# Performance work log

Measured on AMD Instinct MI355X. Metric: run time of the kernel, lower is better.

The kernel has to match this reference:

```python
import jax, jax.numpy as jnp
import numpy as np

B, A, NN, G, F, L, MAXZ = 8, 1024, 64, 25, 128, 3, 100
CUTOFF = 5.0

def ssp(x):
    # shifted softplus: ln(0.5*e^x + 0.5) = softplus(x) - ln(2)
    return jax.nn.softplus(x) - jnp.log(2.0)

def setup_inputs() -> dict:
    key = jax.random.key(0)
    ks = jax.random.split(key, 10)
    atomic_numbers = jax.random.randint(ks[0], (B, A), 0, MAXZ)
    positions = jax.random.normal(ks[1], (B, A, 3), dtype=jnp.float32) * 3.0
    cell = jnp.zeros((B, 3, 3), dtype=jnp.float32)
    cell_offset = jnp.zeros((B, A, NN, 3), dtype=jnp.float32)
    neighbors = jax.random.randint(ks[2], (B, A, NN), 0, A)
    neighbor_mask = jnp.ones((B, A, NN), dtype=jnp.float32)
    s = 0.05
    emb = jax.random.normal(ks[3], (MAXZ, F), dtype=jnp.float32) * s
    emb = emb.at[0].set(0.0)  # padding_idx=0
    return dict(
        atomic_numbers=atomic_numbers, positions=positions, cell=cell,
        cell_offset=cell_offset, neighbors=neighbors, neighbor_mask=neighbor_mask,
        emb=emb,
        fw1=jax.random.normal(ks[4], (L, G, F), dtype=jnp.float32) * s,
        fb1=jnp.zeros((L, F), dtype=jnp.float32),
        fw2=jax.random.normal(ks[5], (L, F, F), dtype=jnp.float32) * s,
        fb2=jnp.zeros((L, F), dtype=jnp.float32),
        in2f_w=jax.random.normal(ks[6], (L, F, F), dtype=jnp.float32) * s,
        f2out_w=jax.random.normal(ks[7], (L, F, F), dtype=jnp.float32) * s,
        f2out_b=jnp.zeros((L, F), dtype=jnp.float32),
        dense_w=jax.random.normal(ks[8], (L, F, F), dtype=jnp.float32) * s,
        dense_b=jnp.zeros((L, F), dtype=jnp.float32),
    )

def reference(atomic_numbers, positions, cell, cell_offset, neighbors,
              neighbor_mask, emb, fw1, fb1, fw2, fb2, in2f_w, f2out_w,
              f2out_b, dense_w, dense_b):
    bidx = jnp.arange(B)[:, None, None]
    # embedding lookup [B,A,F]
    x = emb[atomic_numbers]
    # AtomDistances: gather neighbor positions, add cell offsets, norm
    pos_j = positions[bidx, neighbors]                       # [B,A,NN,3]
    dv = pos_j - positions[:, :, None, :] + jnp.einsum('bank,bkc->banc', cell_offset, cell)
    d2 = jnp.sum(dv * dv, axis=-1)                           # [B,A,NN]
    r_ij = jnp.where(d2 > 0, jnp.sqrt(jnp.where(d2 > 0, d2, 1.0)), 0.0)
    # GaussianSmearing on [0, cutoff] with G gaussians
    offsets = jnp.linspace(0.0, CUTOFF, G)
    width = offsets[1] - offsets[0]
    coeff = -0.5 / (width * width)
    f_ij = jnp.exp(coeff * (r_ij[..., None] - offsets) ** 2)  # [B,A,NN,G]
    mask = neighbor_mask[..., None]                           # [B,A,NN,1]
    for l in range(L):
        # filter-generating network on expanded distances -> [B,A,NN,F]
        W = ssp(f_ij @ fw1[l] + fb1[l]) @ fw2[l] + fb2[l]
        # cfconv: in2f (no bias), gather neighbor features, mul, masked sum
        y = x @ in2f_w[l]                                     # [B,A,F]
        yj = y[bidx, neighbors]                               # [B,A,NN,F]
        v = jnp.sum(yj * W * mask, axis=2)                    # [B,A,F]
        v = ssp(v @ f2out_w[l] + f2out_b[l])
        # interaction output dense (linear)
        v = v @ dense_w[l] + dense_b[l]
        x = x + v
    return x
```

## Files before the change

kernel.cpp:

```cpp
#include <hip/hip_runtime.h>
#include <hip/hip_bf16.h>
#include <math.h>

#define B_ 8
#define A_ 1024
#define NN_ 64
#define G_ 25
#define F_ 128
#define L_ 3
#define TG_ 4096

typedef __hip_bfloat16 bf16;
typedef __bf16 bf16x8 __attribute__((ext_vector_type(8)));
typedef __bf16 bf16x4 __attribute__((ext_vector_type(4)));
typedef float floatx4 __attribute__((ext_vector_type(4)));
#define MFMA16 __builtin_amdgcn_mfma_f32_16x16x32_bf16

__device__ __forceinline__ float sspfast(float x){
  return __logf(0.5f*__expf(x) + 0.5f);
}
__device__ __forceinline__ float ldsel(const void* p, long long i, int isbf){
  return isbf ? __bfloat162float(((const bf16*)p)[i]) : ((const float*)p)[i];
}
__device__ __forceinline__ int sniff_bf16(const void* pos){
  const unsigned* raw = (const unsigned*)pos;
  unsigned w = raw[threadIdx.x & 63];
  unsigned e = (w >> 7) & 0xFF;
  return __popcll(__ballot(e >= 118 && e <= 132)) >= 32;
}

__global__ __launch_bounds__(256) void k_setup(
    const void* emb, const void* fb1, const void* fb2, const void* f2ob,
    const void* db,  const void* fw1, const void* fw2, const void* f2ow,
    const void* dw,  const void* in2f, const void* pos,
    float* c_emb, float* c_fb1, float* c_fb2, float* c_f2ob, float* c_db,
    __bf16* fw1tb, __bf16* fw2tb, __bf16* f2owtb, __bf16* dwtb, __bf16* in2ftb)
{
  int isbf = sniff_bf16(pos);
  int idx = blockIdx.x*256 + threadIdx.x;
  if(idx < 12800){ c_emb[idx] = ldsel(emb, idx, isbf); return; }
  if(idx < 13184){ c_fb1[idx-12800] = ldsel(fb1, idx-12800, isbf); return; }
  if(idx < 13568){ c_fb2[idx-13184] = ldsel(fb2, idx-13184, isbf); return; }
  if(idx < 13952){ c_f2ob[idx-13568] = ldsel(f2ob, idx-13568, isbf); return; }
  if(idx < 14336){ c_db[idx-13952] = ldsel(db, idx-13952, isbf); return; }
  if(idx < 26624){
    int i = idx - 14336;
    int l = i >> 12; int rem = i & 4095; int f = rem >> 5; int k = rem & 31;
    float v = (k < G_) ? ldsel(fw1, (long long)l*G_*F_ + k*F_ + f, isbf) : 0.0f;
    fw1tb[i] = (__bf16)v;
    return;
  }
  {
    int i = idx - 26624;
    int which = i / 49152; int r = i - which*49152;
    int l = r >> 14; int rem = r & 16383; int f = rem >> 7; int k = rem & 127;
    const void* src = (which==0) ? fw2 : (which==1) ? f2ow : (which==2) ? dw : in2f;
    __bf16* dst = (which==0) ? fw2tb : (which==1) ? f2owtb : (which==2) ? dwtb : in2ftb;
    dst[r] = (__bf16)ldsel(src, (long long)l*F_*F_ + k*F_ + f, isbf);
  }
}

__global__ __launch_bounds__(256, 4) void k_build(
    const __bf16* __restrict__ fw1tb, const float* __restrict__ fb1g,
    const __bf16* __restrict__ fw2tb, const float* __restrict__ fb2g,
    __bf16* __restrict__ wtabb,
    const int* __restrict__ z, const float* __restrict__ c_emb,
    const __bf16* __restrict__ in2ftb, float* __restrict__ xws,
    __bf16* __restrict__ ybf,
    const void* pos, const void* cell, const void* celloff,
    const int* __restrict__ nbr, const void* maskg,
    int4* __restrict__ pair)
{
  __shared__ __align__(16) unsigned char smem[22528];
  int t = threadIdx.x;
  int lane = t & 63, wid = t >> 6, c = lane & 15, quad = lane >> 4;
  int wb = wid*32;

  if(blockIdx.x >= 448){
    int isbf = sniff_bf16(pos);
    int p = (blockIdx.x - 448)*256 + t;
    int m = p >> 6;
    int b = m >> 10;
    int j = nbr[p];
    long long pi = (long long)m*3, pj = (long long)(b*A_+j)*3;
    long long co = (long long)p*3, ce = (long long)b*9;
    float o0 = ldsel(celloff,co+0,isbf), o1 = ldsel(celloff,co+1,isbf), o2 = ldsel(celloff,co+2,isbf);
    float d2 = 0.0f;
    #pragma unroll
    for(int cc=0;cc<3;cc++){
      float off = o0*ldsel(cell,ce+cc,isbf) + o1*ldsel(cell,ce+3+cc,isbf) + o2*ldsel(cell,ce+6+cc,isbf);
      float dv = ldsel(pos,pj+cc,isbf) - ldsel(pos,pi+cc,isbf) + off;
      d2 += dv*dv;
    }
    float r = (d2 > 0.0f) ? sqrtf(d2) : 0.0f;
    float msk = ldsel(maskg, p, isbf);
    int i = (int)(r * ((float)TG_ / 8.0f) + 0.5f);
    if(i > TG_-1) i = TG_-1;
    int4 pr;
    pr.x = i * F_;
    pr.y = (b*A_ + j) * F_;
    pr.z = __float_as_int(msk);
    pr.w = 0;
    pair[p] = pr;
    return;
  }

  if(blockIdx.x < 192){
    __bf16* s_h1  = (__bf16*)smem;
    __bf16* s_fij = (__bf16*)(smem + 17408);
    int layer = blockIdx.x >> 6;
    int row0  = (blockIdx.x & 63) * 64;

    const float dr = 8.0f / (float)TG_;
    const float width = 5.0f/24.0f;
    const float coeff = -0.5f/(width*width);
    for(int i=t;i<NN_*40;i+=256){
      int n = i/40, g = i - n*40;
      float val = 0.0f;
      if(g < G_){
        float rg = (float)(row0 + n) * dr;
        float d = rg - (float)g*width;
        val = __expf(coeff*d*d);
      }
      s_fij[i] = (__bf16)val;
    }
    __syncthreads();

    {
      const __bf16* fw1l = fw1tb + layer*F_*32;
      bf16x8 a0 = *(const bf16x8*)(fw1l + (wb + c)*32 + quad*8);
      bf16x8 a1 = *(const bf16x8*)(fw1l + (wb + 16 + c)*32 + quad*8);
      floatx4 bias0 = *(const floatx4*)(fb1g + layer*F_ + wb + quad*4);
      floatx4 bias1 = *(const floatx4*)(fb1g + layer*F_ + wb + 16 + quad*4);
      #pragma unroll
      for(int nt=0;nt<4;nt++){
        bf16x8 bfr = *(const bf16x8*)(s_fij + (nt*16 + c)*40 + quad*8);
        floatx4 z4 = {0.f,0.f,0.f,0.f};
        floatx4 acc0 = MFMA16(a0, bfr, z4, 0,0,0);
        floatx4 acc1 = MFMA16(a1, bfr, z4, 0,0,0);
        bf16x4 h0, h1v;
        #pragma unroll
        for(int r=0;r<4;r++){
          h0[r]  = (__bf16)sspfast(acc0[r] + bias0[r]);
          h1v[r] = (__bf16)sspfast(acc1[r] + bias1[r]);
        }
        *(bf16x4*)(s_h1 + (nt*16+c)*136 + wb + quad*4)      = h0;
        *(bf16x4*)(s_h1 + (nt*16+c)*136 + wb + 16 + quad*4) = h1v;
      }
    }
    __syncthreads();

    {
      const __bf16* fw2l = fw2tb + layer*F_*F_;
      bf16x8 aw0[4], aw1[4];
      #pragma unroll
      for(int kt=0;kt<4;kt++){
        aw0[kt] = *(const bf16x8*)(fw2l + (wb + c)*F_ + kt*32 + quad*8);
        aw1[kt] = *(const bf16x8*)(fw2l + (wb + 16 + c)*F_ + kt*32 + quad*8);
      }
      floatx4 ba0 = *(const floatx4*)(fb2g + layer*F_ + wb + quad*4);
      floatx4 ba1 = *(const floatx4*)(fb2g + layer*F_ + wb + 16 + quad*4);
      __bf16* T = wtabb + (long long)layer*TG_*F_;
      #pragma unroll
      for(int nt=0; nt<4; nt++){
        bf16x8 bh[4];
        #pragma unroll
        for(int kt=0;kt<4;kt++)
          bh[kt] = *(const bf16x8*)(s_h1 + (nt*16 + c)*136 + kt*32 + quad*8);
        floatx4 acc0 = {0.f,0.f,0.f,0.f};
        floatx4 acc1 = {0.f,0.f,0.f,0.f};
        #pragma unroll
        for(int kt=0;kt<4;kt++){
          acc0 = MFMA16(aw0[kt], bh[kt], acc0, 0,0,0);
          acc1 = MFMA16(aw1[kt], bh[kt], acc1, 0,0,0);
        }
        int row = row0 + nt*16 + c;
        bf16x4 o0, o1;
        #pragma unroll
        for(int r=0;r<4;r++){
          o0[r] = (__bf16)(acc0[r] + ba0[r]);
          o1[r] = (__bf16)(acc1[r] + ba1[r]);
        }
        *(bf16x4*)(T + (long long)row*F_ + wb + quad*4)      = o0;
        *(bf16x4*)(T + (long long)row*F_ + wb + 16 + quad*4) = o1;
      }
    }
    return;
  }

  {
    __bf16* s_a = (__bf16*)smem;
    int row0 = (blockIdx.x - 192)*32;
    #pragma unroll
    for(int i=0;i<2;i++){
      int ch = t + i*256, row = ch >> 4, col8 = ch & 15;
      const float* src = c_emb + (long long)z[row0+row]*F_ + col8*8;
      float4 a4 = ((const float4*)src)[0];
      float4 b4 = ((const float4*)src)[1];
      float* xd = xws + (long long)(row0+row)*F_ + col8*8;
      ((float4*)xd)[0] = a4; ((float4*)xd)[1] = b4;
      bf16x8 v = {(__bf16)a4.x,(__bf16)a4.y,(__bf16)a4.z,(__bf16)a4.w,
                  (__bf16)b4.x,(__bf16)b4.y,(__bf16)b4.z,(__bf16)b4.w};
      *(bf16x8*)(s_a + row*136 + col8*8) = v;
    }
    __syncthreads();
    bf16x8 aw0[4], aw1[4];
    #pragma unroll
    for(int kt=0;kt<4;kt++){
      aw0[kt] = *(const bf16x8*)(in2ftb + (wb + c)*F_ + kt*32 + quad*8);
      aw1[kt] = *(const bf16x8*)(in2ftb + (wb + 16 + c)*F_ + kt*32 + quad*8);
    }
    #pragma unroll
    for(int nt=0; nt<2; nt++){
      bf16x8 bh[4];
      #pragma unroll
      for(int kt=0;kt<4;kt++)
        bh[kt] = *(const bf16x8*)(s_a + (nt*16 + c)*136 + kt*32 + quad*8);
      floatx4 acc0 = {0.f,0.f,0.f,0.f};
      floatx4 acc1 = {0.f,0.f,0.f,0.f};
      #pragma unroll
      for(int kt=0;kt<4;kt++){
        acc0 = MFMA16(aw0[kt], bh[kt], acc0, 0,0,0);
        acc1 = MFMA16(aw1[kt], bh[kt], acc1, 0,0,0);
      }
      int row = row0 + nt*16 + c;
      bf16x4 o0, o1;
      #pragma unroll
      for(int r=0;r<4;r++){ o0[r] = (__bf16)acc0[r]; o1[r] = (__bf16)acc1[r]; }
      *(bf16x4*)(ybf + (long long)row*F_ + wb + quad*4)      = o0;
      *(bf16x4*)(ybf + (long long)row*F_ + wb + 16 + quad*4) = o1;
    }
  }
}

__global__ __launch_bounds__(256, 4) void k_layer(
    const __bf16* __restrict__ yin, const int4* __restrict__ pairg,
    const __bf16* __restrict__ Tb, float* __restrict__ xws,
    const __bf16* __restrict__ f2owl, const float* __restrict__ f2obl,
    const __bf16* __restrict__ dwl,  const float* __restrict__ dbl,
    const __bf16* __restrict__ in2fnext, __bf16* __restrict__ yout,
    void* __restrict__ dout, const void* __restrict__ pos,
    int has_next, int write_out)
{
  __shared__ __align__(16) int4   s_pair[8*NN_];
  __shared__ __align__(16) bf16x4 s_vp[4][8][32];
  __shared__ __align__(16) __bf16 s_ga[16*136];
  __shared__ __align__(16) __bf16 s_gb[16*136];

  int t = threadIdx.x;
  int bid = (int)blockIdx.x;
  int m0 = ((bid & 7) * 128 + (bid >> 3)) * 8;
  int lane = t & 63, wid = t >> 6, c = lane & 15, quad = lane >> 4;
  int fq = t & 31, nh = t >> 5;
  int isbf = sniff_bf16(pos);

  {
    const int4* src = pairg + (long long)m0*NN_;
    for(int i=t;i<8*NN_;i+=256) s_pair[i] = src[i];
  }
  __syncthreads();

  int f4 = fq*4;
  #pragma unroll 2
  for(int a=0;a<8;a++){
    float4 v = {0.f,0.f,0.f,0.f};
    #pragma unroll
    for(int jj=0;jj<8;jj++){
      int4 pr = s_pair[a*NN_ + nh*8 + jj];
      float cm = __int_as_float(pr.z);
      bf16x4 T = *(const bf16x4*)(Tb + pr.x + f4);
      bf16x4 Y = *(const bf16x4*)(yin + pr.y + f4);
      v.x += cm * (float)T[0] * (float)Y[0];
      v.y += cm * (float)T[1] * (float)Y[1];
      v.z += cm * (float)T[2] * (float)Y[2];
      v.w += cm * (float)T[3] * (float)Y[3];
    }
    v.x += __shfl_xor(v.x, 32); v.y += __shfl_xor(v.y, 32);
    v.z += __shfl_xor(v.z, 32); v.w += __shfl_xor(v.w, 32);
    if(lane < 32){
      bf16x4 o = {(__bf16)v.x,(__bf16)v.y,(__bf16)v.z,(__bf16)v.w};
      s_vp[wid][a][lane] = o;
    }
  }
  __syncthreads();
  {
    int a = t >> 5, q = t & 31;
    bf16x4 p0 = s_vp[0][a][q], p1 = s_vp[1][a][q];
    bf16x4 p2 = s_vp[2][a][q], p3 = s_vp[3][a][q];
    bf16x4 o;
    #pragma unroll
    for(int r=0;r<4;r++)
      o[r] = (__bf16)((float)p0[r]+(float)p1[r]+(float)p2[r]+(float)p3[r]);
    *(bf16x4*)(s_ga + a*136 + q*4) = o;
  }
  __syncthreads();

  int wb = wid*32;
  {
    bf16x8 aw0[4], aw1[4];
    #pragma unroll
    for(int kt=0;kt<4;kt++){
      aw0[kt] = *(const bf16x8*)(f2owl + (wb + c)*F_ + kt*32 + quad*8);
      aw1[kt] = *(const bf16x8*)(f2owl + (wb + 16 + c)*F_ + kt*32 + quad*8);
    }
    floatx4 ba0 = *(const floatx4*)(f2obl + wb + quad*4);
    floatx4 ba1 = *(const floatx4*)(f2obl + wb + 16 + quad*4);
    bf16x8 bh[4];
    #pragma unroll
    for(int kt=0;kt<4;kt++)
      bh[kt] = *(const bf16x8*)(s_ga + c*136 + kt*32 + quad*8);
    floatx4 acc0 = {0.f,0.f,0.f,0.f};
    floatx4 acc1 = {0.f,0.f,0.f,0.f};
    #pragma unroll
    for(int kt=0;kt<4;kt++){
      acc0 = MFMA16(aw0[kt], bh[kt], acc0, 0,0,0);
      acc1 = MFMA16(aw1[kt], bh[kt], acc1, 0,0,0);
    }
    bf16x4 o0, o1;
    #pragma unroll
    for(int r=0;r<4;r++){
      o0[r] = (__bf16)sspfast(acc0[r] + ba0[r]);
      o1[r] = (__bf16)sspfast(acc1[r] + ba1[r]);
    }
    *(bf16x4*)(s_gb + c*136 + wb + quad*4)      = o0;
    *(bf16x4*)(s_gb + c*136 + wb + 16 + quad*4) = o1;
  }
  __syncthreads();

  {
    bf16x8 aw0[4], aw1[4];
    #pragma unroll
    for(int kt=0;kt<4;kt++){
      aw0[kt] = *(const bf16x8*)(dwl + (wb + c)*F_ + kt*32 + quad*8);
      aw1[kt] = *(const bf16x8*)(dwl + (wb + 16 + c)*F_ + kt*32 + quad*8);
    }
    floatx4 ba0 = *(const floatx4*)(dbl + wb + quad*4);
    floatx4 ba1 = *(const floatx4*)(dbl + wb + 16 + quad*4);
    bf16x8 bh[4];
    #pragma unroll
    for(int kt=0;kt<4;kt++)
      bh[kt] = *(const bf16x8*)(s_gb + c*136 + kt*32 + quad*8);
    floatx4 acc0 = {0.f,0.f,0.f,0.f};
    floatx4 acc1 = {0.f,0.f,0.f,0.f};
    #pragma unroll
    for(int kt=0;kt<4;kt++){
      acc0 = MFMA16(aw0[kt], bh[kt], acc0, 0,0,0);
      acc1 = MFMA16(aw1[kt], bh[kt], acc1, 0,0,0);
    }
    int rowL = m0 + (c & 7);
    float* xp0 = xws + (long long)rowL*F_ + wb + quad*4;
    float* xp1 = xws + (long long)rowL*F_ + wb + 16 + quad*4;
    float4 x0 = *(const float4*)xp0;
    float4 x1 = *(const float4*)xp1;
    float4 xn0 = {x0.x+acc0[0]+ba0[0], x0.y+acc0[1]+ba0[1],
                  x0.z+acc0[2]+ba0[2], x0.w+acc0[3]+ba0[3]};
    float4 xn1 = {x1.x+acc1[0]+ba1[0], x1.y+acc1[1]+ba1[1],
                  x1.z+acc1[2]+ba1[2], x1.w+acc1[3]+ba1[3]};
    bf16x4 s0 = {(__bf16)xn0.x,(__bf16)xn0.y,(__bf16)xn0.z,(__bf16)xn0.w};
    bf16x4 s1 = {(__bf16)xn1.x,(__bf16)xn1.y,(__bf16)xn1.z,(__bf16)xn1.w};
    *(bf16x4*)(s_ga + c*136 + wb + quad*4)      = s0;
    *(bf16x4*)(s_ga + c*136 + wb + 16 + quad*4) = s1;
    if(c < 8){
      *(float4*)xp0 = xn0;
      *(float4*)xp1 = xn1;
      if(write_out){
        long long gi0 = (long long)rowL*F_ + wb + quad*4;
        long long gi1 = (long long)rowL*F_ + wb + 16 + quad*4;
        if(isbf){
          *(bf16x4*)((bf16*)dout + gi0) = s0;
          *(bf16x4*)((bf16*)dout + gi1) = s1;
        }else{
          *(float4*)((float*)dout + gi0) = xn0;
          *(float4*)((float*)dout + gi1) = xn1;
        }
      }
    }
  }
  if(!has_next) return;
  __syncthreads();

  {
    bf16x8 aw0[4], aw1[4];
    #pragma unroll
    for(int kt=0;kt<4;kt++){
      aw0[kt] = *(const bf16x8*)(in2fnext + (wb + c)*F_ + kt*32 + quad*8);
      aw1[kt] = *(const bf16x8*)(in2fnext + (wb + 16 + c)*F_ + kt*32 + quad*8);
    }
    bf16x8 bh[4];
    #pragma unroll
    for(int kt=0;kt<4;kt++)
      bh[kt] = *(const bf16x8*)(s_ga + c*136 + kt*32 + quad*8);
    floatx4 acc0 = {0.f,0.f,0.f,0.f};
    floatx4 acc1 = {0.f,0.f,0.f,0.f};
    #pragma unroll
    for(int kt=0;kt<4;kt++){
      acc0 = MFMA16(aw0[kt], bh[kt], acc0, 0,0,0);
      acc1 = MFMA16(aw1[kt], bh[kt], acc1, 0,0,0);
    }
    if(c < 8){
      int row = m0 + c;
      bf16x4 o0, o1;
      #pragma unroll
      for(int r=0;r<4;r++){ o0[r] = (__bf16)acc0[r]; o1[r] = (__bf16)acc1[r]; }
      *(bf16x4*)(yout + (long long)row*F_ + wb + quad*4)      = o0;
      *(bf16x4*)(yout + (long long)row*F_ + wb + 16 + quad*4) = o1;
    }
  }
}

extern "C" void kernel_launch(void* const* d_in, const int* in_sizes, int n_in,
                              void* d_out, int out_size, void* d_ws, size_t ws_size,
                              hipStream_t stream){
  const int*  z       = (const int*)d_in[0];
  const void* pos     = d_in[1];
  const void* cell    = d_in[2];
  const void* celloff = d_in[3];
  const int*  nbr     = (const int*)d_in[4];
  const void* mask    = d_in[5];
  const void* emb     = d_in[6];
  const void* fw1     = d_in[7];
  const void* fb1     = d_in[8];
  const void* fw2     = d_in[9];
  const void* fb2     = d_in[10];
  const void* in2f    = d_in[11];
  const void* f2ow    = d_in[12];
  const void* f2ob    = d_in[13];
  const void* dw      = d_in[14];
  const void* db      = d_in[15];

  float* base = (float*)d_ws;
  float* c_emb  = base + 16;
  float* c_fb1  = c_emb + 12800;
  float* c_fb2  = c_fb1 + 384;
  float* c_f2ob = c_fb2 + 384;
  float* c_db   = c_f2ob + 384;
  __bf16* fw1tb  = (__bf16*)(c_db + 384);
  __bf16* fw2tb  = (__bf16*)(base + 20496);
  __bf16* f2owtb = (__bf16*)(base + 45072);
  __bf16* dwtb   = (__bf16*)(base + 69648);
  __bf16* in2ftb = (__bf16*)(base + 94224);
  float*  xws   = base + 118800;
  __bf16* ybf0  = (__bf16*)(base + 1167376);
  __bf16* ybf1  = (__bf16*)(base + 1691664);
  int4*   pair  = (int4*)(base + 2215952);
  __bf16* wtabb = (__bf16*)(base + 4313104);

  k_setup<<<872, 256, 0, stream>>>(emb, fb1, fb2, f2ob, db,
                                   fw1, fw2, f2ow, dw, in2f, pos,
                                   c_emb, c_fb1, c_fb2, c_f2ob, c_db,
                                   fw1tb, fw2tb, f2owtb, dwtb, in2ftb);
  k_build<<<2496, 256, 0, stream>>>(fw1tb, c_fb1, fw2tb, c_fb2, wtabb,
                                    z, c_emb, in2ftb, xws, ybf0,
                                    pos, cell, celloff, nbr, mask, pair);

  __bf16* ycur = ybf0;
  __bf16* ynext = ybf1;
  for(int l=0;l<L_;l++){
    k_layer<<<(B_*A_)/8, 256, 0, stream>>>(ycur, pair,
                                           wtabb + (long long)l*TG_*F_, xws,
                                           f2owtb + l*F_*F_, c_f2ob + l*F_,
                                           dwtb + l*F_*F_,  c_db + l*F_,
                                           in2ftb + (l < L_-1 ? (l+1)*F_*F_ : 0), ynext,
                                           d_out, pos,
                                           (l < L_-1) ? 1 : 0, (l == L_-1) ? 1 : 0);
    __bf16* tmp = ycur; ycur = ynext; ynext = tmp;
  }
}
```

Baseline: 192.9 us.

## Shrink pair records, fold mask into zero table row, widen gather loads

Pair records shrink from int4 to int2 by dropping the mask float. Masked-out neighbors now point to an extra zeroed row appended to each filter table, so the multiply by the mask goes away. The gather loop changes from 4-wide to 8-wide bf16 loads with 16 lanes per atom row, reduced by two cross-lane shuffles. Partial sums are kept in fp32 in shared memory instead of bf16, and the unused rows of s_ga are now zeroed explicitly. This cuts pair-buffer traffic and the number of load instructions, at the cost of a larger shared-memory footprint per block.

New measurement: 178.9 us. 7.2% less time.

```diff
diff --git a/kernel.cpp b/kernel.cpp
--- a/kernel.cpp
+++ b/kernel.cpp
@@ -9,6 +9,7 @@
 #define F_ 128
 #define L_ 3
 #define TG_ 4096
+#define TGP_ (TG_ + 8)
 
 typedef __hip_bfloat16 bf16;
 typedef __bf16 bf16x8 __attribute__((ext_vector_type(8)));
@@ -69,7 +70,7 @@
     __bf16* __restrict__ ybf,
     const void* pos, const void* cell, const void* celloff,
     const int* __restrict__ nbr, const void* maskg,
-    int4* __restrict__ pair)
+    int2* __restrict__ pair)
 {
   __shared__ __align__(16) unsigned char smem[22528];
   int t = threadIdx.x;
@@ -96,11 +97,10 @@
     float msk = ldsel(maskg, p, isbf);
     int i = (int)(r * ((float)TG_ / 8.0f) + 0.5f);
     if(i > TG_-1) i = TG_-1;
-    int4 pr;
+    if(msk < 0.5f) i = TG_;
+    int2 pr;
     pr.x = i * F_;
     pr.y = (b*A_ + j) * F_;
-    pr.z = __float_as_int(msk);
-    pr.w = 0;
     pair[p] = pr;
     return;
   }
@@ -110,6 +110,10 @@
     __bf16* s_fij = (__bf16*)(smem + 17408);
     int layer = blockIdx.x >> 6;
     int row0  = (blockIdx.x & 63) * 64;
+    __bf16* T = wtabb + (long long)layer*TGP_*F_;
+
+    if((blockIdx.x & 63) == 0 && t < F_)
+      T[(long long)TG_*F_ + t] = (__bf16)0.0f;
 
     const float dr = 8.0f / (float)TG_;
     const float width = 5.0f/24.0f;
@@ -160,7 +164,6 @@
       }
       floatx4 ba0 = *(const floatx4*)(fb2g + layer*F_ + wb + quad*4);
       floatx4 ba1 = *(const floatx4*)(fb2g + layer*F_ + wb + 16 + quad*4);
-      __bf16* T = wtabb + (long long)layer*TG_*F_;
       #pragma unroll
       for(int nt=0; nt<4; nt++){
         bf16x8 bh[4];
@@ -234,7 +237,7 @@
 }
 
 __global__ __launch_bounds__(256, 4) void k_layer(
-    const __bf16* __restrict__ yin, const int4* __restrict__ pairg,
+    const __bf16* __restrict__ yin, const int2* __restrict__ pairg,
     const __bf16* __restrict__ Tb, float* __restrict__ xws,
     const __bf16* __restrict__ f2owl, const float* __restrict__ f2obl,
     const __bf16* __restrict__ dwl,  const float* __restrict__ dbl,
@@ -242,8 +245,8 @@
     void* __restrict__ dout, const void* __restrict__ pos,
     int has_next, int write_out)
 {
-  __shared__ __align__(16) int4   s_pair[8*NN_];
-  __shared__ __align__(16) bf16x4 s_vp[4][8][32];
+  __shared__ __align__(16) int2  s_pair[8*NN_];
+  __shared__ __align__(16) float s_vpf[4*8*128];
   __shared__ __align__(16) __bf16 s_ga[16*136];
   __shared__ __align__(16) __bf16 s_gb[16*136];
 
@@ -251,47 +254,63 @@
   int bid = (int)blockIdx.x;
   int m0 = ((bid & 7) * 128 + (bid >> 3)) * 8;
   int lane = t & 63, wid = t >> 6, c = lane & 15, quad = lane >> 4;
-  int fq = t & 31, nh = t >> 5;
   int isbf = sniff_bf16(pos);
 
   {
-    const int4* src = pairg + (long long)m0*NN_;
+    const int2* src = pairg + (long long)m0*NN_;
     for(int i=t;i<8*NN_;i+=256) s_pair[i] = src[i];
   }
   __syncthreads();
 
-  int f4 = fq*4;
+  int fsl = t & 15;
+  int grp = t >> 4;
+  int f8 = fsl*8;
   #pragma unroll 2
   for(int a=0;a<8;a++){
-    float4 v = {0.f,0.f,0.f,0.f};
-    #pragma unroll
-    for(int jj=0;jj<8;jj++){
-      int4 pr = s_pair[a*NN_ + nh*8 + jj];
-      float cm = __int_as_float(pr.z);
-      bf16x4 T = *(const bf16x4*)(Tb + pr.x + f4);
-      bf16x4 Y = *(const bf16x4*)(yin + pr.y + f4);
-      v.x += cm * (float)T[0] * (float)Y[0];
-      v.y += cm * (float)T[1] * (float)Y[1];
-      v.z += cm * (float)T[2] * (float)Y[2];
-      v.w += cm * (float)T[3] * (float)Y[3];
-    }
-    v.x += __shfl_xor(v.x, 32); v.y += __shfl_xor(v.y, 32);
-    v.z += __shfl_xor(v.z, 32); v.w += __shfl_xor(v.w, 32);
-    if(lane < 32){
-      bf16x4 o = {(__bf16)v.x,(__bf16)v.y,(__bf16)v.z,(__bf16)v.w};
-      s_vp[wid][a][lane] = o;
+    float v0=0.f,v1=0.f,v2=0.f,v3=0.f,v4=0.f,v5=0.f,v6=0.f,v7=0.f;
+    #pragma unroll
+    for(int jj=0;jj<4;jj++){
+      int2 pr = s_pair[a*NN_ + jj*16 + grp];
+      bf16x8 T = *(const bf16x8*)(Tb + pr.x + f8);
+      bf16x8 Y = *(const bf16x8*)(yin + pr.y + f8);
+      v0 += (float)T[0]*(float)Y[0];
+      v1 += (float)T[1]*(float)Y[1];
+      v2 += (float)T[2]*(float)Y[2];
+      v3 += (float)T[3]*(float)Y[3];
+      v4 += (float)T[4]*(float)Y[4];
+      v5 += (float)T[5]*(float)Y[5];
+      v6 += (float)T[6]*(float)Y[6];
+      v7 += (float)T[7]*(float)Y[7];
+    }
+    v0 += __shfl_xor(v0,16); v1 += __shfl_xor(v1,16);
+    v2 += __shfl_xor(v2,16); v3 += __shfl_xor(v3,16);
+    v4 += __shfl_xor(v4,16); v5 += __shfl_xor(v5,16);
+    v6 += __shfl_xor(v6,16); v7 += __shfl_xor(v7,16);
+    v0 += __shfl_xor(v0,32); v1 += __shfl_xor(v1,32);
+    v2 += __shfl_xor(v2,32); v3 += __shfl_xor(v3,32);
+    v4 += __shfl_xor(v4,32); v5 += __shfl_xor(v5,32);
+    v6 += __shfl_xor(v6,32); v7 += __shfl_xor(v7,32);
+    if(lane < 16){
+      float* dst = s_vpf + (wid*8 + a)*128 + lane*8;
+      floatx4 lo = {v0,v1,v2,v3}, hi = {v4,v5,v6,v7};
+      *(floatx4*)dst = lo;
+      *(floatx4*)(dst+4) = hi;
     }
   }
   __syncthreads();
   {
     int a = t >> 5, q = t & 31;
-    bf16x4 p0 = s_vp[0][a][q], p1 = s_vp[1][a][q];
-    bf16x4 p2 = s_vp[2][a][q], p3 = s_vp[3][a][q];
+    floatx4 p0 = *(const floatx4*)(s_vpf + (0*8+a)*128 + q*4);
+    floatx4 p1 = *(const floatx4*)(s_vpf + (1*8+a)*128 + q*4);
+    floatx4 p2 = *(const floatx4*)(s_vpf + (2*8+a)*128 + q*4);
+    floatx4 p3 = *(const floatx4*)(s_vpf + (3*8+a)*128 + q*4);
     bf16x4 o;
     #pragma unroll
     for(int r=0;r<4;r++)
-      o[r] = (__bf16)((float)p0[r]+(float)p1[r]+(float)p2[r]+(float)p3[r]);
+      o[r] = (__bf16)(p0[r]+p1[r]+p2[r]+p3[r]);
     *(bf16x4*)(s_ga + a*136 + q*4) = o;
+    bf16x4 zz = {(__bf16)0.f,(__bf16)0.f,(__bf16)0.f,(__bf16)0.f};
+    *(bf16x4*)(s_ga + (8+a)*136 + q*4) = zz;
   }
   __syncthreads();
 
@@ -442,8 +461,8 @@
   float*  xws   = base + 118800;
   __bf16* ybf0  = (__bf16*)(base + 1167376);
   __bf16* ybf1  = (__bf16*)(base + 1691664);
-  int4*   pair  = (int4*)(base + 2215952);
-  __bf16* wtabb = (__bf16*)(base + 4313104);
+  int2*   pair  = (int2*)(base + 2215952);
+  __bf16* wtabb = (__bf16*)(base + 3264528);
 
   k_setup<<<872, 256, 0, stream>>>(emb, fb1, fb2, f2ob, db,
                                    fw1, fw2, f2ow, dw, in2f, pos,
@@ -457,7 +476,7 @@
   __bf16* ynext = ybf1;
   for(int l=0;l<L_;l++){
     k_layer<<<(B_*A_)/8, 256, 0, stream>>>(ycur, pair,
-                                           wtabb + (long long)l*TG_*F_, xws,
+                                           wtabb + (long long)l*TGP_*F_, xws,
                                            f2owtb + l*F_*F_, c_f2ob + l*F_,
                                            dwtb + l*F_*F_,  c_db + l*F_,
                                            in2ftb + (l < L_-1 ? (l+1)*F_*F_ : 0), ynext,
```
